# Optimization experiments

Measured on AMD Instinct MI355X. Metric: run time of the kernel, lower is better.

Reference implementation:

```python
import jax, jax.numpy as jnp
import numpy as np

N, F, H, C = 8192, 256, 256, 40
LP = 0.2  # LeakyReLU slope


def setup_inputs() -> dict:
    key = jax.random.key(0)
    ks = jax.random.split(key, 11)
    s = 1.0 / np.sqrt(F)
    return {
        "x": jax.random.normal(ks[0], (N, F), jnp.float32),
        "adj_f": jax.random.uniform(ks[1], (N, N), jnp.float32) / N,
        "adj_a": jax.random.uniform(ks[2], (N, N), jnp.float32) / N,
        "Wp": jax.random.normal(ks[3], (F, F), jnp.float32) * s,
        "bp": jax.random.normal(ks[4], (F,), jnp.float32) * s,
        "Wg": jax.random.normal(ks[5], (F, F), jnp.float32) * s,
        "Wb": jax.random.normal(ks[6], (F, F), jnp.float32) * s,
        "W1": jax.random.normal(ks[7], (F, H), jnp.float32) * s,
        "b1": jax.random.normal(ks[8], (H,), jnp.float32) * s,
        "W2": jax.random.normal(ks[9], (H, C), jnp.float32) * s,
        "b2": jax.random.normal(ks[10], (C,), jnp.float32) * s,
    }


def reference(x, adj_f, adj_a, Wp, bp, Wg, Wb, W1, b1, W2, b2):
    # --- DynamicPrompt.forward ---
    # GraphConvolution: adj_f @ (x @ Wp) + bp, then ReLU
    base_prompt = jax.nn.relu(adj_f @ (x @ Wp) + bp)  # [N, F]
    # adj_a.fill_diagonal_(0)
    idx = jnp.arange(N)
    adj_a0 = adj_a.at[idx, idx].set(0.0)
    neighbor = adj_a0 @ x                             # [N, F]
    gamma = jax.nn.leaky_relu(neighbor @ Wg, LP) + 1.0
    beta = jax.nn.leaky_relu(neighbor @ Wb, LP)
    learned_prompt = gamma * base_prompt + beta
    # F.normalize: L2 along dim=1, eps=1e-12
    nrm = jnp.linalg.norm(learned_prompt, axis=1, keepdims=True)
    learned_prompt = learned_prompt / jnp.maximum(nrm, 1e-12)
    # --- mix prompt into input, run frozen teacher GCN (eval: no dropout) ---
    x_in = 0.5 * (x + learned_prompt)
    h = jax.nn.relu(adj_a @ (x_in @ W1) + b1)         # gc1
    logits = adj_a @ (h @ W2) + b2                    # gc2
    return jax.nn.log_softmax(logits, axis=1)         # [N, C]
```

## Files before the change

### kernel.cpp

```cpp
#include <hip/hip_runtime.h>

typedef unsigned short u16;
typedef __attribute__((ext_vector_type(8))) short bf16x8;
typedef __attribute__((ext_vector_type(4))) float f32x4;

__device__ __forceinline__ u16 f2bf(float f) {
  union { float f; unsigned u; } v; v.f = f;
  unsigned r = v.u + 0x7FFFu + ((v.u >> 16) & 1u);
  return (u16)(r >> 16);
}
__device__ __forceinline__ float bf2f(u16 h) {
  union { unsigned u; float f; } v; v.u = ((unsigned)h) << 16; return v.f;
}
__device__ __forceinline__ unsigned pk2(float a, float b) {
  return (unsigned)f2bf(a) | ((unsigned)f2bf(b) << 16);
}
__device__ __forceinline__ unsigned cvtpk(float a, float b) {
  unsigned r;
  asm("v_cvt_pk_bf16_f32 %0, %1, %2" : "=v"(r) : "v"(a), "v"(b));
  return r;
}
__device__ __forceinline__ void gld16(const void* g, void* l) {
  __builtin_amdgcn_global_load_lds(
      (const __attribute__((address_space(1))) unsigned int*)g,
      (__attribute__((address_space(3))) unsigned int*)l, 16, 0, 0);
}

__global__ __launch_bounds__(256)
void prep_w_k(const float* __restrict__ Wp, const float* __restrict__ Wg,
              const float* __restrict__ Wb, const float* __restrict__ W1,
              const float* __restrict__ W2, u16* __restrict__ WpT,
              u16* __restrict__ WgbT, u16* __restrict__ W1T,
              u16* __restrict__ W2T) {
  int z = blockIdx.z;
  const float* in; u16* out; int C = 256;
  if (z == 0) { in = Wp; out = WpT; }
  else if (z == 1) { in = Wg; out = WgbT; }
  else if (z == 2) { in = Wb; out = WgbT + 65536; }
  else if (z == 3) { in = W1; out = W1T; }
  else { in = W2; out = W2T; C = 40; if (blockIdx.x >= 2) return; }
  __shared__ float tile[32][33];
  int tj = blockIdx.x * 32, ti = blockIdx.y * 32;
  int t = threadIdx.x, c = t & 31, r0 = t >> 5;
#pragma unroll
  for (int p = 0; p < 4; ++p) {
    int r = r0 + p * 8;
    tile[r][c] = (tj + c < C) ? in[(size_t)(ti + r) * C + (tj + c)] : 0.f;
  }
  __syncthreads();
#pragma unroll
  for (int p = 0; p < 4; ++p) {
    int rr = r0 + p * 8;
    out[(size_t)(tj + rr) * 256 + (ti + c)] = f2bf(tile[c][rr]);
  }
}

__global__ __launch_bounds__(256)
void prep_x_k(const float* __restrict__ x, u16* __restrict__ xT,
              u16* __restrict__ xbf) {
  __shared__ float tile[32][33];
  int tj = blockIdx.x * 32, ti = blockIdx.y * 32;
  int t = threadIdx.x, c = t & 31, r0 = t >> 5;
#pragma unroll
  for (int p = 0; p < 4; ++p) {
    int r = r0 + p * 8;
    float v = x[(size_t)(ti + r) * 256 + (tj + c)];
    tile[r][c] = v;
    xbf[(size_t)(ti + r) * 256 + (tj + c)] = f2bf(v);
  }
  __syncthreads();
#pragma unroll
  for (int p = 0; p < 4; ++p) {
    int rr = r0 + p * 8;
    xT[(size_t)(tj + rr) * 8192 + (ti + c)] = f2bf(tile[c][rr]);
  }
}

__global__ __launch_bounds__(256)
void diag_k(const float* __restrict__ adj, float* __restrict__ d) {
  int i = blockIdx.x * 256 + threadIdx.x;
  d[i] = bf2f(f2bf(adj[(size_t)i * 8193]));
}

template <int BN, bool ABF, bool WRB, bool PACK>
__global__ __launch_bounds__(256, 3)
void bgemm_k(const void* __restrict__ Av, const u16* __restrict__ Bt,
             void* __restrict__ part, u16* __restrict__ Aout) {
  constexpr int BM = 64;
  constexpr int KP = 1024;
  constexpr int NSTEP = KP / 64;
  constexpr int MT = 8192 / BM;
  constexpr int AROWB = ABF ? 128 : 256;
  constexpr int ABYTES = BM * AROWB;
  constexpr int NA = ABYTES / 4096;
  constexpr int NB = BN * 128 / 4096;
  constexpr int FR = 2;
  constexpr int FC = BN / 32;

  __shared__ char sA[ABYTES];
  __shared__ u16 sB[BN * 64];
  const int t = threadIdx.x, lane = t & 63, w = t >> 6;
  const int l15 = lane & 15, lhi = lane >> 4;
  const int s = ((blockIdx.x & 7) << 7) | (blockIdx.x >> 3);
  const int kp = s >> 7, m = s & (MT - 1);
  const int mBase = m * BM;
  const int kpBase = kp * KP;
  const int waveM = (w >> 1) * 32;
  const int waveN = (w & 1) * (BN / 2);

  f32x4 acc[FR][FC];
#pragma unroll
  for (int a = 0; a < FR; ++a)
#pragma unroll
    for (int b = 0; b < FC; ++b) acc[a][b] = (f32x4){0.f, 0.f, 0.f, 0.f};

  for (int st = 0; st < NSTEP; ++st) {
    const int k0 = kpBase + st * 64;
#pragma unroll
    for (int i = 0; i < NA; ++i) {
      int L = i * 4096 + t * 16;
      int row, kb;
      if (ABF) { row = L >> 7; kb = (L & 127) ^ ((row & 7) << 4); }
      else     { row = L >> 8; kb = (L & 255) ^ ((row & 7) << 4); }
      const char* g;
      if (ABF)
        g = (const char*)Av + (((size_t)(mBase + row)) << 14) + ((size_t)k0 << 1) + kb;
      else
        g = (const char*)Av + (((size_t)(mBase + row)) << 15) + ((size_t)k0 << 2) + kb;
      gld16(g, (char*)sA + L);
    }
#pragma unroll
    for (int i = 0; i < NB; ++i) {
      int L = i * 4096 + t * 16;
      int n = L >> 7;
      int kb = (L & 127) ^ ((n & 7) << 4);
      gld16((const char*)Bt + ((size_t)n << 14) + ((size_t)k0 << 1) + kb,
            (char*)sB + L);
    }
    __syncthreads();
    if (WRB && !ABF) {
      int r = t >> 2, cb = (t & 3) << 6;
      int sw = (r & 7) << 4;
      const char* sa = (const char*)sA + r * 256;
      f32x4 v0 = *(const f32x4*)(sa + ((cb) ^ sw));
      f32x4 v1 = *(const f32x4*)(sa + ((cb + 16) ^ sw));
      f32x4 v2 = *(const f32x4*)(sa + ((cb + 32) ^ sw));
      f32x4 v3 = *(const f32x4*)(sa + ((cb + 48) ^ sw));
      uint4 q0, q1;
      q0.x = cvtpk(v0.x, v0.y); q0.y = cvtpk(v0.z, v0.w);
      q0.z = cvtpk(v1.x, v1.y); q0.w = cvtpk(v1.z, v1.w);
      q1.x = cvtpk(v2.x, v2.y); q1.y = cvtpk(v2.z, v2.w);
      q1.z = cvtpk(v3.x, v3.y); q1.w = cvtpk(v3.z, v3.w);
      u16* dst = Aout + ((size_t)(mBase + r) << 13) + k0 + (cb >> 2);
      *(uint4*)dst = q0;
      *(uint4*)(dst + 8) = q1;
    }
#pragma unroll
    for (int ks = 0; ks < 2; ++ks) {
      bf16x8 av[FR], bv[FC];
#pragma unroll
      for (int fr = 0; fr < FR; ++fr) {
        int row = waveM + fr * 16 + l15;
        if (ABF) {
          int off = row * 128 + ((ks * 64 + lhi * 16) ^ ((row & 7) << 4));
          av[fr] = *(const bf16x8*)((const char*)sA + off);
        } else {
          int inrow = ks * 128 + lhi * 32;
          int sw = (row & 7) << 4;
          const char* sa = (const char*)sA + row * 256;
          f32x4 x0 = *(const f32x4*)(sa + (inrow ^ sw));
          f32x4 x1 = *(const f32x4*)(sa + ((inrow + 16) ^ sw));
          union { bf16x8 v; unsigned u[4]; } p;
          p.u[0] = cvtpk(x0.x, x0.y); p.u[1] = cvtpk(x0.z, x0.w);
          p.u[2] = cvtpk(x1.x, x1.y); p.u[3] = cvtpk(x1.z, x1.w);
          av[fr] = p.v;
        }
      }
#pragma unroll
      for (int fc = 0; fc < FC; ++fc) {
        int n = waveN + fc * 16 + l15;
        int off = n * 128 + ((ks * 64 + lhi * 16) ^ ((n & 7) << 4));
        bv[fc] = *(const bf16x8*)((const char*)sB + off);
      }
#pragma unroll
      for (int fr = 0; fr < FR; ++fr)
#pragma unroll
        for (int fc = 0; fc < FC; ++fc)
          acc[fr][fc] = __builtin_amdgcn_mfma_f32_16x16x32_bf16(
              av[fr], bv[fc], acc[fr][fc], 0, 0, 0);
    }
    __syncthreads();
  }

  if (PACK) {
    unsigned* pp = (unsigned*)part + (size_t)kp * 8192 * 128 + (size_t)mBase * 128;
#pragma unroll
    for (int fr = 0; fr < FR; ++fr)
#pragma unroll
      for (int fcp = 0; fcp < FC / 2; ++fcp) {
        int g = (waveN >> 5) + fcp;
        int r0 = waveM + fr * 16 + lhi * 4;
#pragma unroll
        for (int j = 0; j < 4; ++j)
          pp[(size_t)(r0 + j) * 128 + g * 16 + l15] =
              cvtpk(acc[fr][2 * fcp][j], acc[fr][2 * fcp + 1][j]);
      }
  } else {
    float* pp = (float*)part + (size_t)kp * 8192 * BN + (size_t)mBase * BN;
#pragma unroll
    for (int fr = 0; fr < FR; ++fr)
#pragma unroll
      for (int fc = 0; fc < FC; ++fc) {
        int col = waveN + fc * 16 + l15;
        int r0 = waveM + fr * 16 + lhi * 4;
#pragma unroll
        for (int j = 0; j < 4; ++j)
          pp[(size_t)(r0 + j) * BN + col] = acc[fr][fc][j];
      }
  }
}

template <int BN, int EPI, int OMODE>
__global__ __launch_bounds__(256)
void sgemm_k(const u16* __restrict__ Abf, const u16* __restrict__ Bt,
             float* __restrict__ C, int ldc, u16* __restrict__ Ct) {
  __shared__ u16 sA[32 * 256];
  __shared__ u16 sB[BN * 256];
  const int t = threadIdx.x, lane = t & 63, w = t >> 6;
  const int rowBase = blockIdx.x * 32;
  const u16* bt = Bt + (size_t)blockIdx.y * BN * 256;
  const int colBlk = blockIdx.y * BN;

#pragma unroll
  for (int i = 0; i < 4; ++i) {
    int lin = ((w * 4 + i) << 10) + (lane << 4);
    int row = lin >> 9;
    int kb = (lin & 511) ^ ((row & 7) << 4);
    const char* g = (const char*)Abf + ((size_t)(rowBase + row) << 9) + kb;
    gld16(g, (char*)sA + ((w * 4 + i) << 10));
  }
#pragma unroll
  for (int i = 0; i < BN / 8; ++i) {
    int lin = ((w * (BN / 8) + i) << 10) + (lane << 4);
    int n = lin >> 9;
    int kb = (lin & 511) ^ ((n & 7) << 4);
    const char* g = (const char*)bt + ((size_t)n << 9) + kb;
    gld16(g, (char*)sB + ((w * (BN / 8) + i) << 10));
  }
  __syncthreads();

  constexpr int FC = BN / 32;
  const int waveM = (w & 1) * 16;
  const int waveN = (w >> 1) * (BN / 2);
  f32x4 acc[FC];
#pragma unroll
  for (int b = 0; b < FC; ++b) acc[b] = (f32x4){0.f, 0.f, 0.f, 0.f};

#pragma unroll
  for (int ks = 0; ks < 8; ++ks) {
    int row = waveM + (lane & 15);
    int offA = (row * 512 + ks * 64 + ((lane >> 4) * 16)) ^ ((row & 7) << 4);
    bf16x8 av = *(const bf16x8*)((const char*)sA + offA);
#pragma unroll
    for (int fc = 0; fc < FC; ++fc) {
      int n = waveN + fc * 16 + (lane & 15);
      int offB = (n * 512 + ks * 64 + ((lane >> 4) * 16)) ^ ((n & 7) << 4);
      bf16x8 bv = *(const bf16x8*)((const char*)sB + offB);
      acc[fc] = __builtin_amdgcn_mfma_f32_16x16x32_bf16(av, bv, acc[fc], 0, 0, 0);
    }
  }

#pragma unroll
  for (int fc = 0; fc < FC; ++fc) {
    int col = waveN + fc * 16 + (lane & 15);
    int r0 = rowBase + waveM + ((lane >> 4) << 2);
    float o[4];
#pragma unroll
    for (int j = 0; j < 4; ++j) {
      float xv = acc[fc][j];
      if (EPI == 1) xv = fmaxf(xv, 0.f);
      if (EPI == 2) xv = (xv > 0.f) ? xv : 0.2f * xv;
      o[j] = xv;
    }
    if (OMODE == 1) {
      uint2 q; q.x = pk2(o[0], o[1]); q.y = pk2(o[2], o[3]);
      *(uint2*)(Ct + (size_t)col * 8192 + r0) = q;
    } else if (OMODE == 2) {
#pragma unroll
      for (int j = 0; j < 4; ++j)
        Ct[(size_t)(r0 + j) * ldc + colBlk + col] = f2bf(o[j]);
    } else {
#pragma unroll
      for (int j = 0; j < 4; ++j)
        C[(size_t)(r0 + j) * ldc + colBlk + col] = o[j];
    }
  }
}

template <int MODE>
__global__ __launch_bounds__(256)
void reduce8p_k(const unsigned* __restrict__ part, const float* __restrict__ bias,
                const float* __restrict__ dd, const u16* __restrict__ xbf,
                u16* __restrict__ Cb) {
  const int tid = threadIdx.x;
  const int row = blockIdx.x * 2 + (tid >> 7);
  const int uc = tid & 127;
  const size_t S = (size_t)8192 * 128;
  const size_t b = (size_t)row * 128 + uc;
  float slo = 0.f, shi = 0.f;
#pragma unroll
  for (int p = 0; p < 8; ++p) {
    unsigned v = part[b + (size_t)p * S];
    slo += bf2f((u16)(v & 0xffff));
    shi += bf2f((u16)(v >> 16));
  }
  const int clo = (uc & 15) + ((uc >> 4) << 5), chi = clo + 16;
  if (MODE == 1) {
    float d = dd[row];
    slo -= d * bf2f(xbf[(size_t)row * 256 + clo]);
    shi -= d * bf2f(xbf[(size_t)row * 256 + chi]);
  } else {
    slo = fmaxf(slo + bias[clo], 0.f);
    shi = fmaxf(shi + bias[chi], 0.f);
  }
  Cb[(size_t)row * 256 + clo] = f2bf(slo);
  Cb[(size_t)row * 256 + chi] = f2bf(shi);
}

__global__ __launch_bounds__(128)
void fuse_red_k(const unsigned* __restrict__ part, const float* __restrict__ bp,
                const u16* __restrict__ gbuf, const u16* __restrict__ xbf,
                u16* __restrict__ xin_bf) {
  const int row = blockIdx.x, uc = threadIdx.x;
  const size_t S = (size_t)8192 * 128;
  const size_t b = (size_t)row * 128 + uc;
  float slo = 0.f, shi = 0.f;
#pragma unroll
  for (int p = 0; p < 8; ++p) {
    unsigned v = part[b + (size_t)p * S];
    slo += bf2f((u16)(v & 0xffff));
    shi += bf2f((u16)(v >> 16));
  }
  const int clo = (uc & 15) + ((uc >> 4) << 5), chi = clo + 16;
  float baselo = fmaxf(slo + bp[clo], 0.f);
  float basehi = fmaxf(shi + bp[chi], 0.f);
  float glo = bf2f(gbuf[(size_t)row * 512 + clo]);
  float ghi = bf2f(gbuf[(size_t)row * 512 + chi]);
  float btlo = bf2f(gbuf[(size_t)row * 512 + 256 + clo]);
  float bthi = bf2f(gbuf[(size_t)row * 512 + 256 + chi]);
  float lplo = (glo + 1.f) * baselo + btlo;
  float lphi = (ghi + 1.f) * basehi + bthi;
  float ss = lplo * lplo + lphi * lphi;
#pragma unroll
  for (int off = 32; off >= 1; off >>= 1) ss += __shfl_xor(ss, off);
  __shared__ float wsum[2];
  if ((uc & 63) == 0) wsum[uc >> 6] = ss;
  __syncthreads();
  float inv = 1.f / fmaxf(sqrtf(wsum[0] + wsum[1]), 1e-12f);
  xin_bf[(size_t)row * 256 + clo] =
      f2bf(0.5f * (bf2f(xbf[(size_t)row * 256 + clo]) + lplo * inv));
  xin_bf[(size_t)row * 256 + chi] =
      f2bf(0.5f * (bf2f(xbf[(size_t)row * 256 + chi]) + lphi * inv));
}

__global__ __launch_bounds__(256)
void reduce_lsm_k(const float* __restrict__ part, const float* __restrict__ b2,
                  float* __restrict__ out) {
  const int t = threadIdx.x, lane = t & 63, w = t >> 6;
  const int row = blockIdx.x * 4 + w;
  const size_t i = (size_t)row * 64 + lane;
  const size_t S = (size_t)8192 * 64;
  float v = 0.f;
#pragma unroll
  for (int p = 0; p < 8; ++p) v += part[i + (size_t)p * S];
  v = (lane < 40) ? v + b2[lane] : -1e30f;
  float mx = v;
#pragma unroll
  for (int off = 32; off >= 1; off >>= 1) mx = fmaxf(mx, __shfl_xor(mx, off));
  float e = (lane < 40) ? expf(v - mx) : 0.f;
#pragma unroll
  for (int off = 32; off >= 1; off >>= 1) e += __shfl_xor(e, off);
  float ls = mx + logf(e);
  if (lane < 40) out[(size_t)row * 40 + lane] = v - ls;
}

extern "C" void kernel_launch(void* const* d_in, const int* in_sizes, int n_in,
                              void* d_out, int out_size, void* d_ws, size_t ws_size,
                              hipStream_t stream) {
  const float* x = (const float*)d_in[0];
  const float* adj_f = (const float*)d_in[1];
  const float* adj_a = (const float*)d_in[2];
  const float* Wp = (const float*)d_in[3];
  const float* bp = (const float*)d_in[4];
  const float* Wg = (const float*)d_in[5];
  const float* Wb = (const float*)d_in[6];
  const float* W1 = (const float*)d_in[7];
  const float* b1 = (const float*)d_in[8];
  const float* W2 = (const float*)d_in[9];
  const float* b2 = (const float*)d_in[10];
  float* out = (float*)d_out;

  char* ws = (char*)d_ws;
  size_t off = 0;
  auto alloc = [&](size_t bytes) {
    char* p = ws + off;
    off += (bytes + 255) & ~(size_t)255;
    return p;
  };
  unsigned* partU = (unsigned*)alloc((size_t)8 * 8192 * 128 * 4);
  float* partF = (float*)partU;
  u16* featT = (u16*)alloc((size_t)256 * 8192 * 2);
  u16* featT64 = (u16*)alloc((size_t)64 * 8192 * 2);
  u16* xT = (u16*)alloc((size_t)256 * 8192 * 2);
  u16* xbf = (u16*)alloc((size_t)8192 * 256 * 2);
  u16* xin_bf = (u16*)alloc((size_t)8192 * 256 * 2);
  u16* neigh_bf = (u16*)alloc((size_t)8192 * 256 * 2);
  u16* h_bf = (u16*)alloc((size_t)8192 * 256 * 2);
  u16* gbuf = (u16*)alloc((size_t)8192 * 512 * 2);
  u16* WpT = (u16*)alloc(256 * 256 * 2);
  u16* WgbT = (u16*)alloc(512 * 256 * 2);
  u16* W1T = (u16*)alloc(256 * 256 * 2);
  u16* W2T = (u16*)alloc(64 * 256 * 2);
  float* dd = (float*)alloc(8192 * 4);

  const size_t adjBytes = (size_t)8192 * 8192 * 2;
  bool useBf = (ws_size >= off + adjBytes + 256);
  u16* adj_bf = useBf ? (u16*)alloc(adjBytes) : nullptr;

  dim3 b256(256);
  prep_w_k<<<dim3(8, 8, 5), b256, 0, stream>>>(Wp, Wg, Wb, W1, W2, WpT, WgbT, W1T, W2T);
  prep_x_k<<<dim3(8, 256), b256, 0, stream>>>(x, xT, xbf);
  diag_k<<<32, b256, 0, stream>>>(adj_a, dd);

  if (useBf)
    bgemm_k<256, false, true, true><<<1024, b256, 0, stream>>>(adj_a, xT, partU, adj_bf);
  else
    bgemm_k<256, false, false, true><<<1024, b256, 0, stream>>>(adj_a, xT, partU, nullptr);
  reduce8p_k<1><<<4096, b256, 0, stream>>>(partU, nullptr, dd, xbf, neigh_bf);
  sgemm_k<256, 2, 2><<<dim3(256, 2), b256, 0, stream>>>(neigh_bf, WgbT, nullptr, 512, gbuf);
  sgemm_k<256, 0, 1><<<dim3(256, 1), b256, 0, stream>>>(xbf, WpT, nullptr, 0, featT);
  bgemm_k<256, false, false, true><<<1024, b256, 0, stream>>>(adj_f, featT, partU, nullptr);
  fuse_red_k<<<8192, dim3(128), 0, stream>>>(partU, bp, gbuf, xbf, xin_bf);
  sgemm_k<256, 0, 1><<<dim3(256, 1), b256, 0, stream>>>(xin_bf, W1T, nullptr, 0, featT);
  if (useBf)
    bgemm_k<256, true, false, true><<<1024, b256, 0, stream>>>(adj_bf, featT, partU, nullptr);
  else
    bgemm_k<256, false, false, true><<<1024, b256, 0, stream>>>(adj_a, featT, partU, nullptr);
  reduce8p_k<2><<<4096, b256, 0, stream>>>(partU, b1, nullptr, nullptr, h_bf);
  sgemm_k<64, 0, 1><<<dim3(256, 1), b256, 0, stream>>>(h_bf, W2T, nullptr, 0, featT64);
  if (useBf)
    bgemm_k<64, true, false, false><<<1024, b256, 0, stream>>>(adj_bf, featT64, partU, nullptr);
  else
    bgemm_k<64, false, false, false><<<1024, b256, 0, stream>>>(adj_a, featT64, partU, nullptr);
  reduce_lsm_k<<<2048, b256, 0, stream>>>(partF, b2, out);
}
```

Measured before the change: 342.4 us.

## Double-buffer adjacency GEMM with 512-thread 128-row tiles, split sgemm columns

The big adjacency GEMM now uses 512-thread blocks covering 128 rows, with double-buffered LDS stages. The next K-slice is prefetched via global_load_lds while MFMAs run on the current slice, replacing the load-then-sync loop. The small feature GEMMs are split into 128-column blocks with twice the grid, which needs a colBlk offset in the transposed output. This costs more LDS per block (only one block per CU) and halves the grid of the big GEMMs, in exchange for overlapping memory traffic with compute.

```diff
diff --git a/kernel.cpp b/kernel.cpp
--- a/kernel.cpp
+++ b/kernel.cpp
@@ -83,26 +83,26 @@
 }
 
 template <int BN, bool ABF, bool WRB, bool PACK>
-__global__ __launch_bounds__(256, 3)
+__global__ __launch_bounds__(512, 1)
 void bgemm_k(const void* __restrict__ Av, const u16* __restrict__ Bt,
              void* __restrict__ part, u16* __restrict__ Aout) {
-  constexpr int BM = 64;
+  constexpr int BM = 128;
   constexpr int KP = 1024;
   constexpr int NSTEP = KP / 64;
   constexpr int MT = 8192 / BM;
   constexpr int AROWB = ABF ? 128 : 256;
   constexpr int ABYTES = BM * AROWB;
-  constexpr int NA = ABYTES / 4096;
-  constexpr int NB = BN * 128 / 4096;
+  constexpr int NA = ABYTES / 8192;
+  constexpr int NB = BN * 128 / 8192;
   constexpr int FR = 2;
   constexpr int FC = BN / 32;
 
-  __shared__ char sA[ABYTES];
-  __shared__ u16 sB[BN * 64];
+  __shared__ char sA[2][ABYTES];
+  __shared__ u16 sB[2][BN * 64];
   const int t = threadIdx.x, lane = t & 63, w = t >> 6;
   const int l15 = lane & 15, lhi = lane >> 4;
-  const int s = ((blockIdx.x & 7) << 7) | (blockIdx.x >> 3);
-  const int kp = s >> 7, m = s & (MT - 1);
+  const int s = ((blockIdx.x & 7) << 6) | (blockIdx.x >> 3);
+  const int kp = s >> 6, m = s & (MT - 1);
   const int mBase = m * BM;
   const int kpBase = kp * KP;
   const int waveM = (w >> 1) * 32;
@@ -114,11 +114,11 @@
 #pragma unroll
     for (int b = 0; b < FC; ++b) acc[a][b] = (f32x4){0.f, 0.f, 0.f, 0.f};
 
-  for (int st = 0; st < NSTEP; ++st) {
-    const int k0 = kpBase + st * 64;
+  auto stage = [&](int buf, int tt) {
+    const int k0 = kpBase + tt * 64;
 #pragma unroll
     for (int i = 0; i < NA; ++i) {
-      int L = i * 4096 + t * 16;
+      int L = i * 8192 + t * 16;
       int row, kb;
       if (ABF) { row = L >> 7; kb = (L & 127) ^ ((row & 7) << 4); }
       else     { row = L >> 8; kb = (L & 255) ^ ((row & 7) << 4); }
@@ -127,25 +127,36 @@
         g = (const char*)Av + (((size_t)(mBase + row)) << 14) + ((size_t)k0 << 1) + kb;
       else
         g = (const char*)Av + (((size_t)(mBase + row)) << 15) + ((size_t)k0 << 2) + kb;
-      gld16(g, (char*)sA + L);
+      gld16(g, (char*)sA[buf] + L);
     }
 #pragma unroll
     for (int i = 0; i < NB; ++i) {
-      int L = i * 4096 + t * 16;
+      int L = i * 8192 + t * 16;
       int n = L >> 7;
       int kb = (L & 127) ^ ((n & 7) << 4);
       gld16((const char*)Bt + ((size_t)n << 14) + ((size_t)k0 << 1) + kb,
-            (char*)sB + L);
-    }
-    __syncthreads();
+            (char*)sB[buf] + L);
+    }
+  };
+
+  stage(0, 0);
+  asm volatile("s_waitcnt vmcnt(0)" ::: "memory");
+  __builtin_amdgcn_s_barrier();
+
+  for (int st = 0; st < NSTEP; ++st) {
+    const int cur = st & 1;
+    if (st + 1 < NSTEP) stage(cur ^ 1, st + 1);
+    const char* sa = (const char*)sA[cur];
+    const char* sb = (const char*)sB[cur];
     if (WRB && !ABF) {
+      const int k0 = kpBase + st * 64;
       int r = t >> 2, cb = (t & 3) << 6;
       int sw = (r & 7) << 4;
-      const char* sa = (const char*)sA + r * 256;
-      f32x4 v0 = *(const f32x4*)(sa + ((cb) ^ sw));
-      f32x4 v1 = *(const f32x4*)(sa + ((cb + 16) ^ sw));
-      f32x4 v2 = *(const f32x4*)(sa + ((cb + 32) ^ sw));
-      f32x4 v3 = *(const f32x4*)(sa + ((cb + 48) ^ sw));
+      const char* sar = sa + r * 256;
+      f32x4 v0 = *(const f32x4*)(sar + ((cb) ^ sw));
+      f32x4 v1 = *(const f32x4*)(sar + ((cb + 16) ^ sw));
+      f32x4 v2 = *(const f32x4*)(sar + ((cb + 32) ^ sw));
+      f32x4 v3 = *(const f32x4*)(sar + ((cb + 48) ^ sw));
       uint4 q0, q1;
       q0.x = cvtpk(v0.x, v0.y); q0.y = cvtpk(v0.z, v0.w);
       q0.z = cvtpk(v1.x, v1.y); q0.w = cvtpk(v1.z, v1.w);
@@ -163,13 +174,13 @@
         int row = waveM + fr * 16 + l15;
         if (ABF) {
           int off = row * 128 + ((ks * 64 + lhi * 16) ^ ((row & 7) << 4));
-          av[fr] = *(const bf16x8*)((const char*)sA + off);
+          av[fr] = *(const bf16x8*)(sa + off);
         } else {
           int inrow = ks * 128 + lhi * 32;
           int sw = (row & 7) << 4;
-          const char* sa = (const char*)sA + row * 256;
-          f32x4 x0 = *(const f32x4*)(sa + (inrow ^ sw));
-          f32x4 x1 = *(const f32x4*)(sa + ((inrow + 16) ^ sw));
+          const char* sar = sa + row * 256;
+          f32x4 x0 = *(const f32x4*)(sar + (inrow ^ sw));
+          f32x4 x1 = *(const f32x4*)(sar + ((inrow + 16) ^ sw));
           union { bf16x8 v; unsigned u[4]; } p;
           p.u[0] = cvtpk(x0.x, x0.y); p.u[1] = cvtpk(x0.z, x0.w);
           p.u[2] = cvtpk(x1.x, x1.y); p.u[3] = cvtpk(x1.z, x1.w);
@@ -180,7 +191,7 @@
       for (int fc = 0; fc < FC; ++fc) {
         int n = waveN + fc * 16 + l15;
         int off = n * 128 + ((ks * 64 + lhi * 16) ^ ((n & 7) << 4));
-        bv[fc] = *(const bf16x8*)((const char*)sB + off);
+        bv[fc] = *(const bf16x8*)(sb + off);
       }
 #pragma unroll
       for (int fr = 0; fr < FR; ++fr)
@@ -189,7 +200,8 @@
           acc[fr][fc] = __builtin_amdgcn_mfma_f32_16x16x32_bf16(
               av[fr], bv[fc], acc[fr][fc], 0, 0, 0);
     }
-    __syncthreads();
+    asm volatile("s_waitcnt vmcnt(0)" ::: "memory");
+    __builtin_amdgcn_s_barrier();
   }
 
   if (PACK) {
@@ -284,7 +296,7 @@
     }
     if (OMODE == 1) {
       uint2 q; q.x = pk2(o[0], o[1]); q.y = pk2(o[2], o[3]);
-      *(uint2*)(Ct + (size_t)col * 8192 + r0) = q;
+      *(uint2*)(Ct + (size_t)(colBlk + col) * 8192 + r0) = q;
     } else if (OMODE == 2) {
 #pragma unroll
       for (int j = 0; j < 4; ++j)
@@ -427,30 +439,30 @@
   bool useBf = (ws_size >= off + adjBytes + 256);
   u16* adj_bf = useBf ? (u16*)alloc(adjBytes) : nullptr;
 
-  dim3 b256(256);
+  dim3 b256(256), b512(512);
   prep_w_k<<<dim3(8, 8, 5), b256, 0, stream>>>(Wp, Wg, Wb, W1, W2, WpT, WgbT, W1T, W2T);
   prep_x_k<<<dim3(8, 256), b256, 0, stream>>>(x, xT, xbf);
   diag_k<<<32, b256, 0, stream>>>(adj_a, dd);
 
   if (useBf)
-    bgemm_k<256, false, true, true><<<1024, b256, 0, stream>>>(adj_a, xT, partU, adj_bf);
+    bgemm_k<256, false, true, true><<<512, b512, 0, stream>>>(adj_a, xT, partU, adj_bf);
   else
-    bgemm_k<256, false, false, true><<<1024, b256, 0, stream>>>(adj_a, xT, partU, nullptr);
+    bgemm_k<256, false, false, true><<<512, b512, 0, stream>>>(adj_a, xT, partU, nullptr);
   reduce8p_k<1><<<4096, b256, 0, stream>>>(partU, nullptr, dd, xbf, neigh_bf);
-  sgemm_k<256, 2, 2><<<dim3(256, 2), b256, 0, stream>>>(neigh_bf, WgbT, nullptr, 512, gbuf);
-  sgemm_k<256, 0, 1><<<dim3(256, 1), b256, 0, stream>>>(xbf, WpT, nullptr, 0, featT);
-  bgemm_k<256, false, false, true><<<1024, b256, 0, stream>>>(adj_f, featT, partU, nullptr);
+  sgemm_k<128, 2, 2><<<dim3(256, 4), b256, 0, stream>>>(neigh_bf, WgbT, nullptr, 512, gbuf);
+  sgemm_k<128, 0, 1><<<dim3(256, 2), b256, 0, stream>>>(xbf, WpT, nullptr, 0, featT);
+  bgemm_k<256, false, false, true><<<512, b512, 0, stream>>>(adj_f, featT, partU, nullptr);
   fuse_red_k<<<8192, dim3(128), 0, stream>>>(partU, bp, gbuf, xbf, xin_bf);
-  sgemm_k<256, 0, 1><<<dim3(256, 1), b256, 0, stream>>>(xin_bf, W1T, nullptr, 0, featT);
+  sgemm_k<128, 0, 1><<<dim3(256, 2), b256, 0, stream>>>(xin_bf, W1T, nullptr, 0, featT);
   if (useBf)
-    bgemm_k<256, true, false, true><<<1024, b256, 0, stream>>>(adj_bf, featT, partU, nullptr);
+    bgemm_k<256, true, false, true><<<512, b512, 0, stream>>>(adj_bf, featT, partU, nullptr);
   else
-    bgemm_k<256, false, false, true><<<1024, b256, 0, stream>>>(adj_a, featT, partU, nullptr);
+    bgemm_k<256, false, false, true><<<512, b512, 0, stream>>>(adj_a, featT, partU, nullptr);
   reduce8p_k<2><<<4096, b256, 0, stream>>>(partU, b1, nullptr, nullptr, h_bf);
   sgemm_k<64, 0, 1><<<dim3(256, 1), b256, 0, stream>>>(h_bf, W2T, nullptr, 0, featT64);
   if (useBf)
-    bgemm_k<64, true, false, false><<<1024, b256, 0, stream>>>(adj_bf, featT64, partU, nullptr);
+    bgemm_k<64, true, false, false><<<512, b512, 0, stream>>>(adj_bf, featT64, partU, nullptr);
   else
-    bgemm_k<64, false, false, false><<<1024, b256, 0, stream>>>(adj_a, featT64, partU, nullptr);
+    bgemm_k<64, false, false, false><<<512, b512, 0, stream>>>(adj_a, featT64, partU, nullptr);
   reduce_lsm_k<<<2048, b256, 0, stream>>>(partF, b2, out);
 }
```

Result: slower. 364.7 us (+6.5%).

## Halve split-K count in big GEMMs, remap XCD tiles, reorder launches

Applied to the files above, without the earlier changes.

The adjacency GEMMs now split K into 4 chunks of 2048 instead of 8 chunks of 1024, launching 512 blocks. Each block is mapped so that blocks on the same XCD share a K chunk and interleave M rows. This halves the partial-sum traffic and the work in the reduction kernels. The small weight GEMMs use 128-column tiles across more grid columns, and the adj_f GEMM is moved ahead of the adj_a path into a separate partial buffer, which changes launch order. The risk is fewer blocks for the GPU's CUs, with longer per-block K loops lowering occupancy and latency hiding.

```diff
diff --git a/kernel.cpp b/kernel.cpp
--- a/kernel.cpp
+++ b/kernel.cpp
@@ -87,9 +87,8 @@
 void bgemm_k(const void* __restrict__ Av, const u16* __restrict__ Bt,
              void* __restrict__ part, u16* __restrict__ Aout) {
   constexpr int BM = 64;
-  constexpr int KP = 1024;
+  constexpr int KP = 2048;
   constexpr int NSTEP = KP / 64;
-  constexpr int MT = 8192 / BM;
   constexpr int AROWB = ABF ? 128 : 256;
   constexpr int ABYTES = BM * AROWB;
   constexpr int NA = ABYTES / 4096;
@@ -101,8 +100,9 @@
   __shared__ u16 sB[BN * 64];
   const int t = threadIdx.x, lane = t & 63, w = t >> 6;
   const int l15 = lane & 15, lhi = lane >> 4;
-  const int s = ((blockIdx.x & 7) << 7) | (blockIdx.x >> 3);
-  const int kp = s >> 7, m = s & (MT - 1);
+  const int xcd = blockIdx.x & 7, idx = blockIdx.x >> 3;
+  const int kp = xcd >> 1;
+  const int m = (idx << 1) | (xcd & 1);
   const int mBase = m * BM;
   const int kpBase = kp * KP;
   const int waveM = (w >> 1) * 32;
@@ -141,11 +141,11 @@
     if (WRB && !ABF) {
       int r = t >> 2, cb = (t & 3) << 6;
       int sw = (r & 7) << 4;
-      const char* sa = (const char*)sA + r * 256;
-      f32x4 v0 = *(const f32x4*)(sa + ((cb) ^ sw));
-      f32x4 v1 = *(const f32x4*)(sa + ((cb + 16) ^ sw));
-      f32x4 v2 = *(const f32x4*)(sa + ((cb + 32) ^ sw));
-      f32x4 v3 = *(const f32x4*)(sa + ((cb + 48) ^ sw));
+      const char* sar = (const char*)sA + r * 256;
+      f32x4 v0 = *(const f32x4*)(sar + ((cb) ^ sw));
+      f32x4 v1 = *(const f32x4*)(sar + ((cb + 16) ^ sw));
+      f32x4 v2 = *(const f32x4*)(sar + ((cb + 32) ^ sw));
+      f32x4 v3 = *(const f32x4*)(sar + ((cb + 48) ^ sw));
       uint4 q0, q1;
       q0.x = cvtpk(v0.x, v0.y); q0.y = cvtpk(v0.z, v0.w);
       q0.z = cvtpk(v1.x, v1.y); q0.w = cvtpk(v1.z, v1.w);
@@ -167,9 +167,9 @@
         } else {
           int inrow = ks * 128 + lhi * 32;
           int sw = (row & 7) << 4;
-          const char* sa = (const char*)sA + row * 256;
-          f32x4 x0 = *(const f32x4*)(sa + (inrow ^ sw));
-          f32x4 x1 = *(const f32x4*)(sa + ((inrow + 16) ^ sw));
+          const char* sar = (const char*)sA + row * 256;
+          f32x4 x0 = *(const f32x4*)(sar + (inrow ^ sw));
+          f32x4 x1 = *(const f32x4*)(sar + ((inrow + 16) ^ sw));
           union { bf16x8 v; unsigned u[4]; } p;
           p.u[0] = cvtpk(x0.x, x0.y); p.u[1] = cvtpk(x0.z, x0.w);
           p.u[2] = cvtpk(x1.x, x1.y); p.u[3] = cvtpk(x1.z, x1.w);
@@ -284,7 +284,7 @@
     }
     if (OMODE == 1) {
       uint2 q; q.x = pk2(o[0], o[1]); q.y = pk2(o[2], o[3]);
-      *(uint2*)(Ct + (size_t)col * 8192 + r0) = q;
+      *(uint2*)(Ct + (size_t)(colBlk + col) * 8192 + r0) = q;
     } else if (OMODE == 2) {
 #pragma unroll
       for (int j = 0; j < 4; ++j)
@@ -299,7 +299,7 @@
 
 template <int MODE>
 __global__ __launch_bounds__(256)
-void reduce8p_k(const unsigned* __restrict__ part, const float* __restrict__ bias,
+void reduce4p_k(const unsigned* __restrict__ part, const float* __restrict__ bias,
                 const float* __restrict__ dd, const u16* __restrict__ xbf,
                 u16* __restrict__ Cb) {
   const int tid = threadIdx.x;
@@ -309,7 +309,7 @@
   const size_t b = (size_t)row * 128 + uc;
   float slo = 0.f, shi = 0.f;
 #pragma unroll
-  for (int p = 0; p < 8; ++p) {
+  for (int p = 0; p < 4; ++p) {
     unsigned v = part[b + (size_t)p * S];
     slo += bf2f((u16)(v & 0xffff));
     shi += bf2f((u16)(v >> 16));
@@ -336,7 +336,7 @@
   const size_t b = (size_t)row * 128 + uc;
   float slo = 0.f, shi = 0.f;
 #pragma unroll
-  for (int p = 0; p < 8; ++p) {
+  for (int p = 0; p < 4; ++p) {
     unsigned v = part[b + (size_t)p * S];
     slo += bf2f((u16)(v & 0xffff));
     shi += bf2f((u16)(v >> 16));
@@ -372,7 +372,7 @@
   const size_t S = (size_t)8192 * 64;
   float v = 0.f;
 #pragma unroll
-  for (int p = 0; p < 8; ++p) v += part[i + (size_t)p * S];
+  for (int p = 0; p < 4; ++p) v += part[i + (size_t)p * S];
   v = (lane < 40) ? v + b2[lane] : -1e30f;
   float mx = v;
 #pragma unroll
@@ -407,8 +407,9 @@
     off += (bytes + 255) & ~(size_t)255;
     return p;
   };
-  unsigned* partU = (unsigned*)alloc((size_t)8 * 8192 * 128 * 4);
-  float* partF = (float*)partU;
+  unsigned* partA = (unsigned*)alloc((size_t)4 * 8192 * 128 * 4);
+  unsigned* partB = (unsigned*)alloc((size_t)4 * 8192 * 128 * 4);
+  float* partBF = (float*)partB;
   u16* featT = (u16*)alloc((size_t)256 * 8192 * 2);
   u16* featT64 = (u16*)alloc((size_t)64 * 8192 * 2);
   u16* xT = (u16*)alloc((size_t)256 * 8192 * 2);
@@ -432,25 +433,25 @@
   prep_x_k<<<dim3(8, 256), b256, 0, stream>>>(x, xT, xbf);
   diag_k<<<32, b256, 0, stream>>>(adj_a, dd);
 
+  sgemm_k<128, 0, 1><<<dim3(256, 2), b256, 0, stream>>>(xbf, WpT, nullptr, 0, featT);
+  bgemm_k<256, false, false, true><<<512, b256, 0, stream>>>(adj_f, featT, partA, nullptr);
   if (useBf)
-    bgemm_k<256, false, true, true><<<1024, b256, 0, stream>>>(adj_a, xT, partU, adj_bf);
+    bgemm_k<256, false, true, true><<<512, b256, 0, stream>>>(adj_a, xT, partB, adj_bf);
   else
-    bgemm_k<256, false, false, true><<<1024, b256, 0, stream>>>(adj_a, xT, partU, nullptr);
-  reduce8p_k<1><<<4096, b256, 0, stream>>>(partU, nullptr, dd, xbf, neigh_bf);
-  sgemm_k<256, 2, 2><<<dim3(256, 2), b256, 0, stream>>>(neigh_bf, WgbT, nullptr, 512, gbuf);
-  sgemm_k<256, 0, 1><<<dim3(256, 1), b256, 0, stream>>>(xbf, WpT, nullptr, 0, featT);
-  bgemm_k<256, false, false, true><<<1024, b256, 0, stream>>>(adj_f, featT, partU, nullptr);
-  fuse_red_k<<<8192, dim3(128), 0, stream>>>(partU, bp, gbuf, xbf, xin_bf);
-  sgemm_k<256, 0, 1><<<dim3(256, 1), b256, 0, stream>>>(xin_bf, W1T, nullptr, 0, featT);
+    bgemm_k<256, false, false, true><<<512, b256, 0, stream>>>(adj_a, xT, partB, nullptr);
+  reduce4p_k<1><<<4096, b256, 0, stream>>>(partB, nullptr, dd, xbf, neigh_bf);
+  sgemm_k<128, 2, 2><<<dim3(256, 4), b256, 0, stream>>>(neigh_bf, WgbT, nullptr, 512, gbuf);
+  fuse_red_k<<<8192, dim3(128), 0, stream>>>(partA, bp, gbuf, xbf, xin_bf);
+  sgemm_k<128, 0, 1><<<dim3(256, 2), b256, 0, stream>>>(xin_bf, W1T, nullptr, 0, featT);
   if (useBf)
-    bgemm_k<256, true, false, true><<<1024, b256, 0, stream>>>(adj_bf, featT, partU, nullptr);
+    bgemm_k<256, true, false, true><<<512, b256, 0, stream>>>(adj_bf, featT, partB, nullptr);
   else
-    bgemm_k<256, false, false, true><<<1024, b256, 0, stream>>>(adj_a, featT, partU, nullptr);
-  reduce8p_k<2><<<4096, b256, 0, stream>>>(partU, b1, nullptr, nullptr, h_bf);
+    bgemm_k<256, false, false, true><<<512, b256, 0, stream>>>(adj_a, featT, partB, nullptr);
+  reduce4p_k<2><<<4096, b256, 0, stream>>>(partB, b1, nullptr, nullptr, h_bf);
   sgemm_k<64, 0, 1><<<dim3(256, 1), b256, 0, stream>>>(h_bf, W2T, nullptr, 0, featT64);
   if (useBf)
-    bgemm_k<64, true, false, false><<<1024, b256, 0, stream>>>(adj_bf, featT64, partU, nullptr);
+    bgemm_k<64, true, false, false><<<512, b256, 0, stream>>>(adj_bf, featT64, partB, nullptr);
   else
-    bgemm_k<64, false, false, false><<<1024, b256, 0, stream>>>(adj_a, featT64, partU, nullptr);
-  reduce_lsm_k<<<2048, b256, 0, stream>>>(partF, b2, out);
-}
+    bgemm_k<64, false, false, false><<<512, b256, 0, stream>>>(adj_a, featT64, partB, nullptr);
+  reduce_lsm_k<<<2048, b256, 0, stream>>>(partBF, b2, out);
+}
```

Measured after the change: 333.9 us (median of 2 runs). 2.5% less time.
